# Optimization experiments

Hardware: AMD Instinct MI355X
Metric: run time of the kernel (lower is better)

Reference implementation:

```python
import jax, jax.numpy as jnp
import numpy as np

ALPHA = 1.0
MIN_FEATURE_SIZE = 1.0
SC = 1e-12                      # stabilizer added to first derivatives
EPS_V_FLOOR = 1e-32 / 6.0       # torch.tensor(1e-32 ** 1 / 6) == 1e-32/6 (** binds tighter than /)


def _grad2d(phi, d):
    """Vectorized equivalent of numerical_gradient_2d: central differences in the
    interior, one-sided forward/backward differences at the boundaries."""
    gx = jnp.concatenate([
        (phi[1:2, :] - phi[0:1, :]) / d,           # forward diff at i == 0
        (phi[2:, :] - phi[:-2, :]) / (2.0 * d),    # central diff in interior
        (phi[-1:, :] - phi[-2:-1, :]) / d,         # backward diff at i == H-1
    ], axis=0)
    gy = jnp.concatenate([
        (phi[:, 1:2] - phi[:, 0:1]) / d,
        (phi[:, 2:] - phi[:, :-2]) / (2.0 * d),
        (phi[:, -1:] - phi[:, -2:-1]) / d,
    ], axis=1)
    return gx, gy


def setup_inputs() -> dict:
    key = jax.random.key(0)
    eps = jax.random.normal(key, (4096, 4096), dtype=jnp.float32)
    grid_size = jnp.asarray(0.05, dtype=jnp.float32)
    return {"eps": eps, "grid_size": grid_size}


def reference(eps, grid_size):
    # mirror the field along axis 1 (torch.cat((eps, eps.flip(1)), dim=1)) -> [H, 2W]
    eps = jnp.concatenate([eps, eps[:, ::-1]], axis=1)

    # ls_derivatives: first derivatives (+SC), then second derivatives of those
    eps_x, eps_y = _grad2d(eps, grid_size)
    eps_x = eps_x + SC
    eps_y = eps_y + SC
    eps_xx, eps_xy = _grad2d(eps_x, grid_size)
    _, eps_yy = _grad2d(eps_y, grid_size)

    pi_d = np.pi / (1.1 * MIN_FEATURE_SIZE)
    eps_v = jnp.maximum(jnp.sqrt(eps_x**2 + eps_y**2), EPS_V_FLOOR)
    k = (eps_x**2 * eps_yy - 2.0 * eps_x * eps_y * eps_xy + eps_y**2 * eps_xx) / eps_v**3
    curve_const = jnp.abs(k * jnp.arctan(eps_v / eps)) - pi_d
    return jnp.nansum(ALPHA * jnp.maximum(curve_const, 0.0) * grid_size**2)
```

## Files before the change

kernel.cpp:

```cpp
#include <hip/hip_runtime.h>
#include <math.h>


#define BLOCK_X 256
#define ROWS_PER 16

__device__ __forceinline__ float fast_atan_ratio(float v, float c, float rv)
{
    const float rc = __builtin_amdgcn_rcpf(c);
    const float q  = v * rc;
    const float iq = c * rv;
    const bool  big = fabsf(q) > 1.0f;
    const float t  = big ? iq : q;
    const float s  = t * t;
    float p = fmaf(s, -0.01172120f, 0.05265332f);
    p = fmaf(s, p, -0.11643287f);
    p = fmaf(s, p,  0.19354346f);
    p = fmaf(s, p, -0.33262347f);
    p = fmaf(s, p,  0.99997726f);
    const float at = p * t;
    const float hp = copysignf(1.57079632679f, q);
    return big ? (hp - at) : at;
}

template<bool YB>
__device__ __forceinline__ float strip_compute(
    const float* __restrict__ eps, int Hn, int Wn, int i0,
    int j, int jm, int jmm, int cjp, int cjpp,
    float rd, float rd2, float syj, float sym, bool jz)
{
    const float SC     = 1e-12f;
    const float FLOORV = (float)(1e-32 / 6.0);
    const float pi_d   = 3.14159265358979323846f / 1.1f;

    auto rp = [&](int t) -> const float* {
        int tt = t;
        if (YB) { tt = tt < 0 ? 0 : tt; tt = tt > Hn - 1 ? Hn - 1 : tt; }
        return eps + (size_t)tt * (size_t)Wn;
    };

    float a2 = rp(i0 - 2)[j],   a1 = rp(i0 - 1)[j],  a0 = rp(i0)[j];
    float b1 = rp(i0 + 1)[j],   b2 = rp(i0 + 2)[j];
    float wN = rp(i0 - 1)[jm],  w0 = rp(i0)[jm],     wS = rp(i0 + 1)[jm];
    float eN = rp(i0 - 1)[cjp], e0 = rp(i0)[cjp],    eS = rp(i0 + 1)[cjp];
    float ww = rp(i0)[jmm],     ee = rp(i0)[cjpp];

    const float* pj = eps + (size_t)(i0 + 3) * (size_t)Wn;
    const float* p2 = eps + (size_t)(i0 + 2) * (size_t)Wn;
    const float* p1 = eps + (size_t)(i0 + 1) * (size_t)Wn;

    float acc = 0.0f;
    #pragma unroll 4
    for (int r = 0; r < ROWS_PER; ++r) {
        const int i = i0 + r;

        float nb2, nwS, neS, nww, nee;
        if (YB) {
            const float* q3 = rp(i + 3);
            const float* q2 = rp(i + 2);
            const float* q1 = rp(i + 1);
            nb2 = q3[j]; nwS = q2[jm]; neS = q2[cjp];
            nww = q1[jmm]; nee = q1[cjpp];
        } else {
            nb2 = pj[j]; nwS = p2[jm]; neS = p2[cjp];
            nww = p1[jmm]; nee = p1[cjpp];
            pj += Wn; p2 += Wn; p1 += Wn;
        }

        float sxi = rd2, sxm = rd2, sxp = rd2;
        bool itop = false, ibot = false;
        if (YB) {
            itop = (i == 0); ibot = (i == Hn - 1);
            sxi = (itop || ibot) ? rd : rd2;
            sxm = (i == 1) ? rd : rd2;
            sxp = (i == Hn - 2) ? rd : rd2;
        }

        const float ex = fmaf(b1 - a1, sxi, SC);
        const float ey = fmaf(e0 - w0, syj, SC);
        float exn = fmaf(a0 - a2, sxm, SC);
        float exs = fmaf(b2 - a0, sxp, SC);
        if (YB) { if (itop) exn = ex; if (ibot) exs = ex; }
        const float exx = (exs - exn) * sxi;
        float eyw = fmaf(a0 - ww, sym, SC);
        const float eye = fmaf(ee - a0, rd2, SC);
        if (jz) eyw = ey;
        const float eyy = (eye - eyw) * syj;
        const float exy = ((eS - eN) - (wS - wN)) * (sxi * syj);

        const float t1 = ex * ex, t2 = ey * ey;
        float num = t1 * eyy;
        num = fmaf(t2, exx, num);
        num = fmaf(-2.0f * (ex * ey), exy, num);
        float ev = __builtin_amdgcn_sqrtf(t1 + t2);
        ev = fmaxf(ev, FLOORV);
        const float rv = __builtin_amdgcn_rcpf(ev);
        const float k  = num * (rv * rv) * rv;
        const float at = fast_atan_ratio(ev, a0, rv);
        const float cc = fabsf(k * at) - pi_d;
        float contrib = fmaxf(cc, 0.0f);
        if (YB && i >= Hn) contrib = 0.0f;
        acc += contrib;

        a2 = a1; a1 = a0; a0 = b1; b1 = b2; b2 = nb2;
        wN = w0; w0 = wS; wS = nwS;
        eN = e0; e0 = eS; eS = neS;
        ww = nww; ee = nee;
    }
    return acc;
}

__global__ __launch_bounds__(BLOCK_X) void curve_partial_kernel(
    const float* __restrict__ eps, const float* __restrict__ gs,
    double* __restrict__ partial, int Hn, int Wn)
{
    const int tx = threadIdx.x;
    const int j  = blockIdx.x * BLOCK_X + tx;
    const int i0 = blockIdx.y * ROWS_PER;
    const float d   = gs[0];
    const float rd  = 1.0f / d;
    const float rd2 = 0.5f * rd;

    const int jm  = (j > 0) ? j - 1 : 0;
    const int jmm = (j > 1) ? j - 2 : 0;
    const int jp = j + 1, jpp = j + 2;
    const int cjp  = (jp  < Wn) ? jp  : (2 * Wn - 1 - jp);
    const int cjpp = (jpp < Wn) ? jpp : (2 * Wn - 1 - jpp);
    const bool jz = (j == 0);
    const float syj = jz ? rd : rd2;
    const float sym = (jm == 0) ? rd : rd2;

    const bool yint = (i0 >= 2) && (i0 + ROWS_PER + 2 < Hn);
    const float accf = yint
        ? strip_compute<false>(eps, Hn, Wn, i0, j, jm, jmm, cjp, cjpp, rd, rd2, syj, sym, jz)
        : strip_compute<true >(eps, Hn, Wn, i0, j, jm, jmm, cjp, cjpp, rd, rd2, syj, sym, jz);

    double acc = (double)accf;
    #pragma unroll
    for (int off = 32; off > 0; off >>= 1)
        acc += __shfl_down(acc, off, 64);
    __shared__ double lds[BLOCK_X / 64];
    const int lane = tx & 63, wv = tx >> 6;
    if (lane == 0) lds[wv] = acc;
    __syncthreads();
    if (tx == 0) {
        partial[blockIdx.y * gridDim.x + blockIdx.x] =
            lds[0] + lds[1] + lds[2] + lds[3];
    }
}

__global__ __launch_bounds__(256) void curve_finish_kernel(
    const double* __restrict__ partial, int n,
    const float* __restrict__ gs, float* __restrict__ out)
{
    const int tx = threadIdx.x;
    double acc = 0.0;
    for (int idx = tx; idx < n; idx += 256) acc += partial[idx];
    #pragma unroll
    for (int off = 32; off > 0; off >>= 1)
        acc += __shfl_down(acc, off, 64);
    __shared__ double lds[4];
    const int lane = tx & 63, wv = tx >> 6;
    if (lane == 0) lds[wv] = acc;
    __syncthreads();
    if (tx == 0) {
        const double dd = (double)gs[0];
        out[0] = (float)((lds[0] + lds[1] + lds[2] + lds[3]) * 2.0 * dd * dd);
    }
}

extern "C" void kernel_launch(void* const* d_in, const int* in_sizes, int n_in,
                              void* d_out, int out_size, void* d_ws, size_t ws_size,
                              hipStream_t stream) {
    const float* eps = (const float*)d_in[0];
    const float* gs  = (const float*)d_in[1];
    float* out = (float*)d_out;

    const int n = in_sizes[0];
    int Wn = (int)(sqrt((double)n) + 0.5);
    int Hn = n / Wn;

    const int gx = (Wn + BLOCK_X - 1) / BLOCK_X;
    const int gy = (Hn + ROWS_PER - 1) / ROWS_PER;
    double* partial = (double*)d_ws;

    curve_partial_kernel<<<dim3(gx, gy), BLOCK_X, 0, stream>>>(eps, gs, partial, Hn, Wn);
    curve_finish_kernel<<<1, 256, 0, stream>>>(partial, gx * gy, gs, out);
}
```

Measured before the change: 115.9 us.

## Process two columns per thread with packed float2 math and vector loads

Each thread now handles two adjacent columns, using 8-byte vector loads of a 6-wide row window and packed float2 arithmetic (which may map to the packed FP32 instructions on CDNA3/4) for the interior strips. Edge blocks use a templated variant with boundary fixups, and strips touching the top or bottom boundary fall back to calling the scalar clamped path twice. The grid is halved in x and launch bounds request 4 blocks per SM. The aim is fewer load instructions and more ALU throughput per element, at the cost of higher register pressure and a grid that assumes the width is divisible by 512.

```diff
diff --git a/kernel.cpp b/kernel.cpp
--- a/kernel.cpp
+++ b/kernel.cpp
@@ -4,6 +4,24 @@
 
 #define BLOCK_X 256
 #define ROWS_PER 16
+
+typedef float f32x2 __attribute__((ext_vector_type(2)));
+
+__device__ __forceinline__ f32x2 mk2(float a, float b) { f32x2 v; v.x = a; v.y = b; return v; }
+__device__ __forceinline__ f32x2 sp2(float a) { return mk2(a, a); }
+
+#if __has_builtin(__builtin_elementwise_fma)
+__device__ __forceinline__ f32x2 fma2(f32x2 a, f32x2 b, f32x2 c) { return __builtin_elementwise_fma(a, b, c); }
+#else
+__device__ __forceinline__ f32x2 fma2(f32x2 a, f32x2 b, f32x2 c) { return mk2(fmaf(a.x, b.x, c.x), fmaf(a.y, b.y, c.y)); }
+#endif
+#if __has_builtin(__builtin_elementwise_max)
+__device__ __forceinline__ f32x2 max2(f32x2 a, f32x2 b) { return __builtin_elementwise_max(a, b); }
+#else
+__device__ __forceinline__ f32x2 max2(f32x2 a, f32x2 b) { return mk2(fmaxf(a.x, b.x), fmaxf(a.y, b.y)); }
+#endif
+__device__ __forceinline__ f32x2 abs2(f32x2 a) { return mk2(fabsf(a.x), fabsf(a.y)); }
+
 
 __device__ __forceinline__ float fast_atan_ratio(float v, float c, float rv)
 {
@@ -23,19 +41,127 @@
     return big ? (hp - at) : at;
 }
 
-template<bool YB>
-__device__ __forceinline__ float strip_compute(
-    const float* __restrict__ eps, int Hn, int Wn, int i0,
-    int j, int jm, int jmm, int cjp, int cjpp,
-    float rd, float rd2, float syj, float sym, bool jz)
+__device__ __forceinline__ f32x2 fast_atan_ratio2(f32x2 v, f32x2 c, f32x2 rvv)
+{
+    const f32x2 rc = mk2(__builtin_amdgcn_rcpf(c.x), __builtin_amdgcn_rcpf(c.y));
+    const f32x2 q  = v * rc;
+    const f32x2 iq = c * rvv;
+    const bool big0 = fabsf(q.x) > 1.0f, big1 = fabsf(q.y) > 1.0f;
+    const f32x2 t = mk2(big0 ? iq.x : q.x, big1 ? iq.y : q.y);
+    const f32x2 s = t * t;
+    f32x2 p = fma2(s, sp2(-0.01172120f), sp2(0.05265332f));
+    p = fma2(s, p, sp2(-0.11643287f));
+    p = fma2(s, p, sp2( 0.19354346f));
+    p = fma2(s, p, sp2(-0.33262347f));
+    p = fma2(s, p, sp2( 0.99997726f));
+    const f32x2 at = p * t;
+    const float hp0 = copysignf(1.57079632679f, q.x);
+    const float hp1 = copysignf(1.57079632679f, q.y);
+    return mk2(big0 ? (hp0 - at.x) : at.x, big1 ? (hp1 - at.y) : at.y);
+}
+
+template<bool XE>
+__device__ __forceinline__ void load6(const float* __restrict__ rowp, int j0,
+                                      bool left, bool right,
+                                      f32x2& m, f32x2& c, f32x2& p)
+{
+    c = *reinterpret_cast<const f32x2*>(rowp + j0);
+    if (XE) {
+        const float* ma = rowp + (left  ? j0 : j0 - 2);
+        const float* pa = rowp + (right ? j0 : j0 + 2);
+        m = *reinterpret_cast<const f32x2*>(ma);
+        p = *reinterpret_cast<const f32x2*>(pa);
+        if (left)  m = mk2(c.x, c.x);
+        if (right) p = mk2(c.y, c.x);
+    } else {
+        m = *reinterpret_cast<const f32x2*>(rowp + j0 - 2);
+        p = *reinterpret_cast<const f32x2*>(rowp + j0 + 2);
+    }
+}
+
+template<bool XE>
+__device__ __forceinline__ f32x2 strip_packed(
+    const float* __restrict__ eps, int Wn, int i0, int j0,
+    bool left, bool right, float rd2, f32x2 syjv, f32x2 symv)
+{
+    const f32x2 SC2    = sp2(1e-12f);
+    const float FLOORV = (float)(1e-32 / 6.0);
+    const float pi_d   = 3.14159265358979323846f / 1.1f;
+
+    const float* r0 = eps + (size_t)(i0 - 2) * (size_t)Wn;
+    f32x2 A = *reinterpret_cast<const f32x2*>(r0 + j0);
+    f32x2 Bm, Bc, Bp, Cm, Cc, Cp, Dm, Dc, Dp, Em, Ec, Ep;
+    load6<XE>(r0 + (size_t)Wn,     j0, left, right, Bm, Bc, Bp);
+    load6<XE>(r0 + (size_t)2 * Wn, j0, left, right, Cm, Cc, Cp);
+    load6<XE>(r0 + (size_t)3 * Wn, j0, left, right, Dm, Dc, Dp);
+    load6<XE>(r0 + (size_t)4 * Wn, j0, left, right, Em, Ec, Ep);
+    const float* pr = r0 + (size_t)5 * Wn;
+
+    f32x2 acc = sp2(0.0f);
+    #pragma unroll 4
+    for (int r = 0; r < ROWS_PER; ++r) {
+        f32x2 Fm, Fc, Fp;
+        load6<XE>(pr, j0, left, right, Fm, Fc, Fp);
+        pr += Wn;
+
+        const f32x2 ex  = fma2(Dc - Bc, sp2(rd2), SC2);
+        const f32x2 Cl1 = mk2(Cm.y, Cc.x), Cr1 = mk2(Cc.y, Cp.x);
+        const f32x2 ey  = fma2(Cr1 - Cl1, syjv, SC2);
+        const f32x2 exn = fma2(Cc - A,  sp2(rd2), SC2);
+        const f32x2 exs = fma2(Ec - Cc, sp2(rd2), SC2);
+        const f32x2 exx = (exs - exn) * rd2;
+        f32x2 eyw = fma2(Cc - Cm, symv, SC2);
+        const f32x2 eye = fma2(Cp - Cc, sp2(rd2), SC2);
+        if (XE) { if (left) eyw.x = ey.x; }
+        const f32x2 eyy = (eye - eyw) * syjv;
+        const f32x2 Bl1 = mk2(Bm.y, Bc.x), Br1 = mk2(Bc.y, Bp.x);
+        const f32x2 Dl1 = mk2(Dm.y, Dc.x), Dr1 = mk2(Dc.y, Dp.x);
+        const f32x2 exy = ((Dr1 - Br1) - (Dl1 - Bl1)) * (syjv * rd2);
+
+        const f32x2 t1 = ex * ex, t2 = ey * ey;
+        f32x2 num = t1 * eyy;
+        num = fma2(t2, exx, num);
+        num = fma2((ex * ey) * -2.0f, exy, num);
+        const f32x2 ssum = t1 + t2;
+        float ev0 = __builtin_amdgcn_sqrtf(ssum.x);
+        float ev1 = __builtin_amdgcn_sqrtf(ssum.y);
+        ev0 = fmaxf(ev0, FLOORV);
+        ev1 = fmaxf(ev1, FLOORV);
+        const f32x2 evv = mk2(ev0, ev1);
+        const f32x2 rvv = mk2(__builtin_amdgcn_rcpf(ev0), __builtin_amdgcn_rcpf(ev1));
+        const f32x2 k   = num * (rvv * rvv) * rvv;
+        const f32x2 at  = fast_atan_ratio2(evv, Cc, rvv);
+        const f32x2 cc  = abs2(k * at) - sp2(pi_d);
+        acc = acc + max2(cc, sp2(0.0f));
+
+        A  = Bc;
+        Bm = Cm; Bc = Cc; Bp = Cp;
+        Cm = Dm; Cc = Dc; Cp = Dp;
+        Dm = Em; Dc = Ec; Dp = Ep;
+        Em = Fm; Ec = Fc; Ep = Fp;
+    }
+    return acc;
+}
+
+__device__ float strip_scalar_yb(const float* __restrict__ eps, int Hn, int Wn,
+                                 int i0, int j, float rd, float rd2)
 {
     const float SC     = 1e-12f;
     const float FLOORV = (float)(1e-32 / 6.0);
     const float pi_d   = 3.14159265358979323846f / 1.1f;
 
+    const int jm  = (j > 0) ? j - 1 : 0;
+    const int jmm = (j > 1) ? j - 2 : 0;
+    const int jp = j + 1, jpp = j + 2;
+    const int cjp  = (jp  < Wn) ? jp  : (2 * Wn - 1 - jp);
+    const int cjpp = (jpp < Wn) ? jpp : (2 * Wn - 1 - jpp);
+    const bool jz = (j == 0);
+    const float syj = jz ? rd : rd2;
+    const float sym = (jm == 0) ? rd : rd2;
+
     auto rp = [&](int t) -> const float* {
-        int tt = t;
-        if (YB) { tt = tt < 0 ? 0 : tt; tt = tt > Hn - 1 ? Hn - 1 : tt; }
+        int tt = t < 0 ? 0 : t;
+        tt = tt > Hn - 1 ? Hn - 1 : tt;
         return eps + (size_t)tt * (size_t)Wn;
     };
 
@@ -45,42 +171,27 @@
     float eN = rp(i0 - 1)[cjp], e0 = rp(i0)[cjp],    eS = rp(i0 + 1)[cjp];
     float ww = rp(i0)[jmm],     ee = rp(i0)[cjpp];
 
-    const float* pj = eps + (size_t)(i0 + 3) * (size_t)Wn;
-    const float* p2 = eps + (size_t)(i0 + 2) * (size_t)Wn;
-    const float* p1 = eps + (size_t)(i0 + 1) * (size_t)Wn;
-
     float acc = 0.0f;
     #pragma unroll 4
     for (int r = 0; r < ROWS_PER; ++r) {
         const int i = i0 + r;
-
-        float nb2, nwS, neS, nww, nee;
-        if (YB) {
-            const float* q3 = rp(i + 3);
-            const float* q2 = rp(i + 2);
-            const float* q1 = rp(i + 1);
-            nb2 = q3[j]; nwS = q2[jm]; neS = q2[cjp];
-            nww = q1[jmm]; nee = q1[cjpp];
-        } else {
-            nb2 = pj[j]; nwS = p2[jm]; neS = p2[cjp];
-            nww = p1[jmm]; nee = p1[cjpp];
-            pj += Wn; p2 += Wn; p1 += Wn;
-        }
-
-        float sxi = rd2, sxm = rd2, sxp = rd2;
-        bool itop = false, ibot = false;
-        if (YB) {
-            itop = (i == 0); ibot = (i == Hn - 1);
-            sxi = (itop || ibot) ? rd : rd2;
-            sxm = (i == 1) ? rd : rd2;
-            sxp = (i == Hn - 2) ? rd : rd2;
-        }
+        const float* q3 = rp(i + 3);
+        const float* q2 = rp(i + 2);
+        const float* q1 = rp(i + 1);
+        const float nb2 = q3[j], nwS = q2[jm], neS = q2[cjp];
+        const float nww = q1[jmm], nee = q1[cjpp];
+
+        const bool itop = (i == 0), ibot = (i == Hn - 1);
+        const float sxi = (itop || ibot) ? rd : rd2;
+        const float sxm = (i == 1) ? rd : rd2;
+        const float sxp = (i == Hn - 2) ? rd : rd2;
 
         const float ex = fmaf(b1 - a1, sxi, SC);
         const float ey = fmaf(e0 - w0, syj, SC);
         float exn = fmaf(a0 - a2, sxm, SC);
         float exs = fmaf(b2 - a0, sxp, SC);
-        if (YB) { if (itop) exn = ex; if (ibot) exs = ex; }
+        if (itop) exn = ex;
+        if (ibot) exs = ex;
         const float exx = (exs - exn) * sxi;
         float eyw = fmaf(a0 - ww, sym, SC);
         const float eye = fmaf(ee - a0, rd2, SC);
@@ -97,9 +208,9 @@
         const float rv = __builtin_amdgcn_rcpf(ev);
         const float k  = num * (rv * rv) * rv;
         const float at = fast_atan_ratio(ev, a0, rv);
-        const float cc = fabsf(k * at) - pi_d;
-        float contrib = fmaxf(cc, 0.0f);
-        if (YB && i >= Hn) contrib = 0.0f;
+        const float ccv = fabsf(k * at) - pi_d;
+        float contrib = fmaxf(ccv, 0.0f);
+        if (i >= Hn) contrib = 0.0f;
         acc += contrib;
 
         a2 = a1; a1 = a0; a0 = b1; b1 = b2; b2 = nb2;
@@ -110,32 +221,35 @@
     return acc;
 }
 
-__global__ __launch_bounds__(BLOCK_X) void curve_partial_kernel(
+__global__ __launch_bounds__(BLOCK_X, 4) void curve_partial_kernel(
     const float* __restrict__ eps, const float* __restrict__ gs,
     double* __restrict__ partial, int Hn, int Wn)
 {
     const int tx = threadIdx.x;
-    const int j  = blockIdx.x * BLOCK_X + tx;
+    const int j0 = (blockIdx.x * BLOCK_X + tx) * 2;
     const int i0 = blockIdx.y * ROWS_PER;
     const float d   = gs[0];
     const float rd  = 1.0f / d;
     const float rd2 = 0.5f * rd;
-
-    const int jm  = (j > 0) ? j - 1 : 0;
-    const int jmm = (j > 1) ? j - 2 : 0;
-    const int jp = j + 1, jpp = j + 2;
-    const int cjp  = (jp  < Wn) ? jp  : (2 * Wn - 1 - jp);
-    const int cjpp = (jpp < Wn) ? jpp : (2 * Wn - 1 - jpp);
-    const bool jz = (j == 0);
-    const float syj = jz ? rd : rd2;
-    const float sym = (jm == 0) ? rd : rd2;
+    const bool left  = (j0 == 0);
+    const bool right = (j0 + 2 == Wn);
 
     const bool yint = (i0 >= 2) && (i0 + ROWS_PER + 2 < Hn);
-    const float accf = yint
-        ? strip_compute<false>(eps, Hn, Wn, i0, j, jm, jmm, cjp, cjpp, rd, rd2, syj, sym, jz)
-        : strip_compute<true >(eps, Hn, Wn, i0, j, jm, jmm, cjp, cjpp, rd, rd2, syj, sym, jz);
-
-    double acc = (double)accf;
+
+    f32x2 accv;
+    if (yint) {
+        const f32x2 syjv = left ? mk2(rd,  rd2) : sp2(rd2);
+        const f32x2 symv = left ? mk2(rd2, rd ) : sp2(rd2);
+        const bool xe = (blockIdx.x == 0) || (blockIdx.x == gridDim.x - 1);
+        accv = xe
+            ? strip_packed<true >(eps, Wn, i0, j0, left, right, rd2, syjv, symv)
+            : strip_packed<false>(eps, Wn, i0, j0, left, right, rd2, syjv, symv);
+    } else {
+        accv.x = strip_scalar_yb(eps, Hn, Wn, i0, j0,     rd, rd2);
+        accv.y = strip_scalar_yb(eps, Hn, Wn, i0, j0 + 1, rd, rd2);
+    }
+
+    double acc = (double)accv.x + (double)accv.y;
     #pragma unroll
     for (int off = 32; off > 0; off >>= 1)
         acc += __shfl_down(acc, off, 64);
@@ -180,7 +294,7 @@
     int Wn = (int)(sqrt((double)n) + 0.5);
     int Hn = n / Wn;
 
-    const int gx = (Wn + BLOCK_X - 1) / BLOCK_X;
+    const int gx = Wn / (BLOCK_X * 2);
     const int gy = (Hn + ROWS_PER - 1) / ROWS_PER;
     double* partial = (double*)d_ws;
 
```

Result: faster. 112.3 us (-3.1%).
